# Optimization experiments

Measured on AMD Instinct MI355X. Metric: run time of the kernel, lower is better.

Reference implementation:

```python
import jax, jax.numpy as jnp
import numpy as np

N_NODES = 50000

def gcn_conv(x, src, dst, W, b, n_nodes):
    # PyG GCNConv: add self-loops, symmetric normalization D^-1/2 (A+I) D^-1/2, then bias
    loop = jnp.arange(n_nodes)
    s = jnp.concatenate([src, loop])
    d = jnp.concatenate([dst, loop])
    deg = jax.ops.segment_sum(jnp.ones(s.shape[0], x.dtype), d, num_segments=n_nodes)
    dinv = jnp.where(deg > 0, jax.lax.rsqrt(deg), 0.0)
    norm = dinv[s] * dinv[d]                      # [E+N]
    h = x @ W                                      # [N, out]
    msg = h[s] * norm[:, None]                     # gather + scale
    out = jax.ops.segment_sum(msg, d, num_segments=n_nodes)  # scatter-add
    return out + b

def setup_inputs() -> dict:
    key = jax.random.key(0)
    ks = jax.random.split(key, 8)
    x = jax.random.normal(ks[0], (N_NODES, 128), jnp.float32)
    edge_index = jax.random.randint(ks[1], (2, 800000), 0, N_NODES)
    def glorot(k, fan_in, fan_out):
        lim = np.sqrt(6.0 / (fan_in + fan_out)).astype(np.float32)
        return jax.random.uniform(k, (fan_in, fan_out), jnp.float32, -lim, lim)
    return {
        "x": x,
        "edge_index": edge_index,
        "conv_w1": glorot(ks[2], 128, 64), "conv_b1": jnp.zeros((64,), jnp.float32),
        "conv_w2": glorot(ks[3], 64, 64),  "conv_b2": jnp.zeros((64,), jnp.float32),
        "fc_w1": glorot(ks[4], 64, 32),    "fc_b1": jnp.zeros((32,), jnp.float32),
        "fc_w2": glorot(ks[5], 32, 1),     "fc_b2": jnp.zeros((1,), jnp.float32),
    }

def reference(x, edge_index, conv_w1, conv_b1, conv_w2, conv_b2, fc_w1, fc_b1, fc_w2, fc_b2):
    src, dst = edge_index[0], edge_index[1]
    h = jnp.tanh(gcn_conv(x, src, dst, conv_w1, conv_b1, N_NODES))
    h = jnp.tanh(gcn_conv(h, src, dst, conv_w2, conv_b2, N_NODES))
    h = jnp.tanh(h @ fc_w1 + fc_b1)  # dropout is identity at inference
    return h @ fc_w2 + fc_b2          # [N, 1]
```

## Files before the change

kernel.cpp:

```cpp
#include <hip/hip_runtime.h>
#include <math.h>

#define TPB 256
#define NBK_MAX 512
#define FILL_CAP 4096
#define SC_CH 16

typedef short bf16x8 __attribute__((ext_vector_type(8)));
typedef float f32x4 __attribute__((ext_vector_type(4)));

__device__ __forceinline__ unsigned short rne_bf16(float f) {
  unsigned u = __float_as_uint(f);
  return (unsigned short)((u + 0x7fffu + ((u >> 16) & 1u)) >> 16);
}
__device__ __forceinline__ float bf16_f(unsigned short v) {
  return __uint_as_float((unsigned)v << 16);
}

__global__ __launch_bounds__(TPB) void k_bcount(const int* __restrict__ dst,
                                                int* __restrict__ btot, int E, int NBK) {
  __shared__ int h[NBK_MAX];
  int tid = threadIdx.x, blk = blockIdx.x, G = gridDim.x;
  for (int b = tid; b < NBK; b += TPB) h[b] = 0;
  __syncthreads();
  int chunk = (E + G - 1) / G, lo = blk * chunk, hi = min(E, lo + chunk);
  for (int e = lo + tid; e < hi; e += TPB) atomicAdd(&h[dst[e] >> 7], 1);
  __syncthreads();
  for (int b = tid; b < NBK; b += TPB)
    if (h[b]) atomicAdd(&btot[b], h[b]);
}

__global__ __launch_bounds__(TPB) void k_bstart(const int* __restrict__ btot,
                                                int* __restrict__ bstart,
                                                int* __restrict__ gcur,
                                                int* __restrict__ rowptr,
                                                int NBK, int N, int E) {
  __shared__ int sc[TPB];
  int t = threadIdx.x;
  int i0 = 2 * t, i1 = 2 * t + 1;
  int a0 = (i0 < NBK) ? btot[i0] : 0;
  int a1 = (i1 < NBK) ? btot[i1] : 0;
  int s = a0 + a1;
  sc[t] = s;
  __syncthreads();
  for (int o = 1; o < TPB; o <<= 1) {
    int v = (t >= o) ? sc[t - o] : 0;
    __syncthreads();
    sc[t] += v;
    __syncthreads();
  }
  int excl = sc[t] - s;
  if (i0 < NBK) { bstart[i0] = excl;      gcur[i0] = excl; }
  if (i1 < NBK) { bstart[i1] = excl + a0; gcur[i1] = excl + a0; }
  if (t == 0) { bstart[NBK] = E; rowptr[N] = E; }
}

__global__ __launch_bounds__(TPB) void k_bscatter(const int* __restrict__ src,
                                                  const int* __restrict__ dst,
                                                  int* __restrict__ gcur,
                                                  unsigned* __restrict__ e2,
                                                  int E, int NBK) {
  __shared__ int h[NBK_MAX];
  __shared__ int base[NBK_MAX];
  int tid = threadIdx.x, blk = blockIdx.x, G = gridDim.x;
  int chunk = (E + G - 1) / G, lo = blk * chunk, hi = min(E, lo + chunk);
  for (int t0 = lo; t0 < hi; t0 += TPB * SC_CH) {
    int sv[SC_CH], dv[SC_CH];
    for (int b = tid; b < NBK; b += TPB) h[b] = 0;
    __syncthreads();
#pragma unroll
    for (int u = 0; u < SC_CH; ++u) {
      int e = t0 + u * TPB + tid;
      if (e < hi) {
        dv[u] = dst[e];
        sv[u] = src[e];
        atomicAdd(&h[dv[u] >> 7], 1);
      } else {
        dv[u] = -1;
      }
    }
    __syncthreads();
    for (int b = tid; b < NBK; b += TPB) {
      int c = h[b];
      base[b] = c ? atomicAdd(&gcur[b], c) : 0;
    }
    __syncthreads();
    for (int b = tid; b < NBK; b += TPB) h[b] = 0;
    __syncthreads();
#pragma unroll
    for (int u = 0; u < SC_CH; ++u) {
      if (dv[u] >= 0) {
        int bk = dv[u] >> 7;
        int r = atomicAdd(&h[bk], 1);
        e2[base[bk] + r] = ((unsigned)sv[u] << 7) | (unsigned)(dv[u] & 127);
      }
    }
    __syncthreads();
  }
}

__global__ __launch_bounds__(TPB) void k_build(const unsigned* __restrict__ e2,
                                               const int* __restrict__ bstart,
                                               int* __restrict__ rowptr,
                                               float* __restrict__ dinv,
                                               int* __restrict__ col, int N) {
  __shared__ int c[128], sc[128], cur[128];
  __shared__ int buf[FILL_CAP];
  int tid = threadIdx.x, b = blockIdx.x;
  int st = bstart[b], en = bstart[b + 1], len = en - st;
  if (tid < 128) c[tid] = 0;
  __syncthreads();
  for (int i = st + tid; i < en; i += TPB) atomicAdd(&c[e2[i] & 127u], 1);
  __syncthreads();
  if (tid < 128) sc[tid] = c[tid];
  __syncthreads();
  for (int o = 1; o < 128; o <<= 1) {
    int v = (tid >= o && tid < 128) ? sc[tid - o] : 0;
    __syncthreads();
    if (tid < 128) sc[tid] += v;
    __syncthreads();
  }
  if (tid < 128) {
    int excl = sc[tid] - c[tid];
    cur[tid] = excl;
    int node = b * 128 + tid;
    if (node < N) {
      rowptr[node] = st + excl;
      dinv[node] = rsqrtf((float)(c[tid] + 1));
    }
  }
  __syncthreads();
  if (len <= FILL_CAP) {
    for (int i = st + tid; i < en; i += TPB) {
      unsigned v = e2[i];
      int p = atomicAdd(&cur[v & 127u], 1);
      buf[p] = (int)(v >> 7);
    }
    __syncthreads();
    for (int i = tid; i < len; i += TPB) col[st + i] = buf[i];
  } else {
    for (int i = st + tid; i < en; i += TPB) {
      unsigned v = e2[i];
      int p = atomicAdd(&cur[v & 127u], 1);
      col[st + p] = (int)(v >> 7);
    }
  }
}

__global__ __launch_bounds__(TPB) void k_wsplit2(const float* __restrict__ W1,
                                                 const float* __restrict__ W2,
                                                 unsigned short* __restrict__ hi1,
                                                 unsigned short* __restrict__ lo1,
                                                 unsigned short* __restrict__ hi2,
                                                 unsigned short* __restrict__ lo2) {
  int i = blockIdx.x * TPB + threadIdx.x;
  if (i < 128 * 64) {
    int k = i >> 6, n = i & 63;
    float w = W1[i];
    unsigned short h = rne_bf16(w);
    hi1[n * 128 + k] = h;
    lo1[n * 128 + k] = rne_bf16(w - bf16_f(h));
  } else if (i < 128 * 64 + 64 * 64) {
    int j = i - 128 * 64;
    int k = j >> 6, n = j & 63;
    float w = W2[j];
    unsigned short h = rne_bf16(w);
    hi2[n * 64 + k] = h;
    lo2[n * 64 + k] = rne_bf16(w - bf16_f(h));
  }
}

template <int K, bool AF32>
__global__ __launch_bounds__(TPB) void k_mm(const void* __restrict__ Ap,
                                            const unsigned short* __restrict__ WThi,
                                            const unsigned short* __restrict__ WTlo,
                                            unsigned short* __restrict__ Hout, int N) {
  constexpr int P = K + 8;
  __shared__ unsigned short sHi[64 * P];
  __shared__ unsigned short sLo[64 * P];
  int tid = threadIdx.x;
  constexpr int CH = 64 * K / 8;
  for (int i = tid; i < CH; i += TPB) {
    int n = i / (K / 8), ko = i % (K / 8);
    *(int4*)(sHi + n * P + ko * 8) = *(const int4*)(WThi + n * K + ko * 8);
    *(int4*)(sLo + n * P + ko * 8) = *(const int4*)(WTlo + n * K + ko * 8);
  }
  __syncthreads();
  int wave = tid >> 6, lane = tid & 63;
  int oct = lane >> 4, l15 = lane & 15;
  int base = blockIdx.x * 64 + wave * 16;
  int arow = base + l15;
  if (arow >= N) arow = N - 1;
  f32x4 acc[4] = {};
#pragma unroll
  for (int s = 0; s < K / 32; ++s) {
    bf16x8 ahi, alo;
    if (AF32) {
      const float* ap = (const float*)Ap + (size_t)arow * K + s * 32 + oct * 8;
      float4 f0 = *(const float4*)ap;
      float4 f1 = *(const float4*)(ap + 4);
      float fv[8] = {f0.x, f0.y, f0.z, f0.w, f1.x, f1.y, f1.z, f1.w};
#pragma unroll
      for (int j = 0; j < 8; ++j) {
        unsigned short hb = rne_bf16(fv[j]);
        ahi[j] = (short)hb;
        alo[j] = (short)rne_bf16(fv[j] - bf16_f(hb));
      }
    } else {
      ahi = *(const bf16x8*)((const unsigned short*)Ap + (size_t)arow * K + s * 32 + oct * 8);
    }
#pragma unroll
    for (int t = 0; t < 4; ++t) {
      bf16x8 bhi = *(const bf16x8*)(sHi + (t * 16 + l15) * P + s * 32 + oct * 8);
      bf16x8 blo = *(const bf16x8*)(sLo + (t * 16 + l15) * P + s * 32 + oct * 8);
      acc[t] = __builtin_amdgcn_mfma_f32_16x16x32_bf16(ahi, bhi, acc[t], 0, 0, 0);
      acc[t] = __builtin_amdgcn_mfma_f32_16x16x32_bf16(ahi, blo, acc[t], 0, 0, 0);
      if (AF32)
        acc[t] = __builtin_amdgcn_mfma_f32_16x16x32_bf16(alo, bhi, acc[t], 0, 0, 0);
    }
  }
#pragma unroll
  for (int r = 0; r < 4; ++r) {
    int row = base + oct * 4 + r;
    if (row < N) {
#pragma unroll
      for (int t = 0; t < 4; ++t)
        Hout[(size_t)row * 64 + t * 16 + l15] = rne_bf16(acc[t][r]);
    }
  }
}

__device__ __forceinline__ float rl_f(float v, int l) {
  return __int_as_float(__builtin_amdgcn_readlane(__float_as_int(v), l));
}

__global__ __launch_bounds__(TPB) void k_agg(const unsigned short* __restrict__ H,
                                             const int* __restrict__ rowptr,
                                             const int* __restrict__ col,
                                             const float* __restrict__ dinv,
                                             const float* __restrict__ bias,
                                             unsigned short* __restrict__ OUT, int N) {
  int i = (blockIdx.x * TPB + threadIdx.x) >> 6;
  int lane = threadIdx.x & 63;
  if (i >= N) return;
  float di = dinv[i];
  float acc = bf16_f(H[((size_t)i << 6) + lane]) * di * di;
  int beg = rowptr[i], end = rowptr[i + 1];
  for (int c0 = beg; c0 < end; c0 += 64) {
    int m = end - c0;
    if (m > 64) m = 64;
    int jj = c0 + lane;
    int sv = col[jj < end ? jj : beg];
    float nv = di * dinv[sv];
    int t = 0;
    for (; t + 8 <= m; t += 8) {
      int s0 = __builtin_amdgcn_readlane(sv, t + 0);
      int s1 = __builtin_amdgcn_readlane(sv, t + 1);
      int s2 = __builtin_amdgcn_readlane(sv, t + 2);
      int s3 = __builtin_amdgcn_readlane(sv, t + 3);
      int s4 = __builtin_amdgcn_readlane(sv, t + 4);
      int s5 = __builtin_amdgcn_readlane(sv, t + 5);
      int s6 = __builtin_amdgcn_readlane(sv, t + 6);
      int s7 = __builtin_amdgcn_readlane(sv, t + 7);
      float h0 = bf16_f(H[((size_t)s0 << 6) + lane]);
      float h1 = bf16_f(H[((size_t)s1 << 6) + lane]);
      float h2 = bf16_f(H[((size_t)s2 << 6) + lane]);
      float h3 = bf16_f(H[((size_t)s3 << 6) + lane]);
      float h4 = bf16_f(H[((size_t)s4 << 6) + lane]);
      float h5 = bf16_f(H[((size_t)s5 << 6) + lane]);
      float h6 = bf16_f(H[((size_t)s6 << 6) + lane]);
      float h7 = bf16_f(H[((size_t)s7 << 6) + lane]);
      acc += h0 * rl_f(nv, t + 0);
      acc += h1 * rl_f(nv, t + 1);
      acc += h2 * rl_f(nv, t + 2);
      acc += h3 * rl_f(nv, t + 3);
      acc += h4 * rl_f(nv, t + 4);
      acc += h5 * rl_f(nv, t + 5);
      acc += h6 * rl_f(nv, t + 6);
      acc += h7 * rl_f(nv, t + 7);
    }
    if (t + 4 <= m) {
      int s0 = __builtin_amdgcn_readlane(sv, t + 0);
      int s1 = __builtin_amdgcn_readlane(sv, t + 1);
      int s2 = __builtin_amdgcn_readlane(sv, t + 2);
      int s3 = __builtin_amdgcn_readlane(sv, t + 3);
      float h0 = bf16_f(H[((size_t)s0 << 6) + lane]);
      float h1 = bf16_f(H[((size_t)s1 << 6) + lane]);
      float h2 = bf16_f(H[((size_t)s2 << 6) + lane]);
      float h3 = bf16_f(H[((size_t)s3 << 6) + lane]);
      acc += h0 * rl_f(nv, t + 0);
      acc += h1 * rl_f(nv, t + 1);
      acc += h2 * rl_f(nv, t + 2);
      acc += h3 * rl_f(nv, t + 3);
      t += 4;
    }
    for (; t < m; ++t) {
      int s = __builtin_amdgcn_readlane(sv, t);
      acc += bf16_f(H[((size_t)s << 6) + lane]) * rl_f(nv, t);
    }
  }
  acc += bias[lane];
  OUT[((size_t)i << 6) + lane] = rne_bf16(tanhf(acc));
}

__global__ __launch_bounds__(TPB) void k_fc(const unsigned short* __restrict__ A,
                                            const float* __restrict__ w1,
                                            const float* __restrict__ b1,
                                            const float* __restrict__ w2,
                                            const float* __restrict__ b2,
                                            float* __restrict__ out, int N) {
  __shared__ float sw1t[32 * 64];
  __shared__ float sb1[32];
  __shared__ float sw2[32];
  __shared__ float sA[128 * 65];
  int tid = threadIdx.x;
  for (int i = tid; i < 32 * 64; i += TPB) {
    int j = i >> 6, k = i & 63;
    sw1t[i] = w1[k * 32 + j];
  }
  if (tid < 32) { sb1[tid] = b1[tid]; sw2[tid] = w2[tid]; }
  int base = blockIdx.x * 128;
  for (int i = tid; i < 128 * 64; i += TPB) {
    int r = i >> 6, c = i & 63;
    int g = base + r;
    sA[r * 65 + c] = (g < N) ? bf16_f(A[(size_t)g * 64 + c]) : 0.f;
  }
  __syncthreads();
  int r = tid >> 1, q = tid & 1;
  int node = base + r;
  const float* arow = &sA[r * 65];
  float o = 0.f;
  for (int j = q * 16; j < q * 16 + 16; ++j) {
    float accj = sb1[j];
    const float* wrow = &sw1t[j * 64];
#pragma unroll 8
    for (int k = 0; k < 64; ++k) accj += arow[k] * wrow[k];
    o += tanhf(accj) * sw2[j];
  }
  o += __shfl_xor(o, 1);
  if (q == 0 && node < N) out[node] = o + b2[0];
}

extern "C" void kernel_launch(void* const* d_in, const int* in_sizes, int n_in,
                              void* d_out, int out_size, void* d_ws, size_t ws_size,
                              hipStream_t stream) {
  const float* x   = (const float*)d_in[0];
  const int*   ei  = (const int*)d_in[1];
  const float* w1  = (const float*)d_in[2];
  const float* b1  = (const float*)d_in[3];
  const float* w2  = (const float*)d_in[4];
  const float* b2  = (const float*)d_in[5];
  const float* fw1 = (const float*)d_in[6];
  const float* fb1 = (const float*)d_in[7];
  const float* fw2 = (const float*)d_in[8];
  const float* fb2 = (const float*)d_in[9];
  float* out = (float*)d_out;

  int N = in_sizes[0] / 128;
  int E = in_sizes[1] / 2;
  const int* src = ei;
  const int* dst = ei + E;

  const int G   = 256;
  const int NBK = (N + 127) / 128;

  char* p = (char*)d_ws;
  size_t off = 0;
  auto take = [&](size_t bytes) -> void* {
    void* r = p + off;
    off += (bytes + 255) & ~(size_t)255;
    return r;
  };
  int*            btot   = (int*)take((size_t)NBK * 4);
  int*            bstart = (int*)take((size_t)(NBK + 1) * 4);
  int*            gcur   = (int*)take((size_t)NBK * 4);
  int*            rowptr = (int*)take((size_t)(N + 1) * 4);
  float*          dinv   = (float*)take((size_t)N * 4);
  unsigned*       e2     = (unsigned*)take((size_t)E * 4);
  int*            col    = (int*)take((size_t)E * 4);
  unsigned short* wt1hi  = (unsigned short*)take(64 * 128 * 2);
  unsigned short* wt1lo  = (unsigned short*)take(64 * 128 * 2);
  unsigned short* wt2hi  = (unsigned short*)take(64 * 64 * 2);
  unsigned short* wt2lo  = (unsigned short*)take(64 * 64 * 2);
  unsigned short* h      = (unsigned short*)take((size_t)N * 64 * 2);
  unsigned short* a      = (unsigned short*)take((size_t)N * 64 * 2);
  (void)ws_size; (void)n_in; (void)out_size;

  hipMemsetAsync(btot, 0, (size_t)NBK * 4, stream);
  k_bcount<<<G, TPB, 0, stream>>>(dst, btot, E, NBK);
  k_bstart<<<1, TPB, 0, stream>>>(btot, bstart, gcur, rowptr, NBK, N, E);
  k_bscatter<<<G, TPB, 0, stream>>>(src, dst, gcur, e2, E, NBK);
  k_build<<<NBK, TPB, 0, stream>>>(e2, bstart, rowptr, dinv, col, N);

  k_wsplit2<<<48, TPB, 0, stream>>>(w1, w2, wt1hi, wt1lo, wt2hi, wt2lo);

  int gmm = (N + 63) / 64;
  k_mm<128, true><<<gmm, TPB, 0, stream>>>(x, wt1hi, wt1lo, h, N);
  k_agg<<<(N + 3) / 4, TPB, 0, stream>>>(h, rowptr, col, dinv, b1, a, N);
  k_mm<64, false><<<gmm, TPB, 0, stream>>>(a, wt2hi, wt2lo, h, N);
  k_agg<<<(N + 3) / 4, TPB, 0, stream>>>(h, rowptr, col, dinv, b2, a, N);
  k_fc<<<(N + 127) / 128, TPB, 0, stream>>>(a, fw1, fb1, fw2, fb2, out, N);
}
```

Before: 218.2 us.

## Fuse weight split into matmul, vectorize aggregation gather, fuse FC head into second aggregation

Removes the separate weight-split kernel: each matmul block now converts the fp32 weights to bf16 hi/lo pairs directly into shared memory. The aggregation kernel is restructured so each lane loads 4 bf16 features (8 bytes) and the wave handles 4 edges per step, followed by a cross-lane shuffle reduction. The second aggregation now runs as a persistent grid that also computes the FC layers, so the separate k_fc kernel and one intermediate write/read disappear. The costs are redundant weight conversion in every matmul block, extra shuffles, and per-group __syncthreads in the fused kernel.

```diff
diff --git a/kernel.cpp b/kernel.cpp
--- a/kernel.cpp
+++ b/kernel.cpp
@@ -16,6 +16,8 @@
 __device__ __forceinline__ float bf16_f(unsigned short v) {
   return __uint_as_float((unsigned)v << 16);
 }
+__device__ __forceinline__ float blo(unsigned u) { return __uint_as_float(u << 16); }
+__device__ __forceinline__ float bhi(unsigned u) { return __uint_as_float(u & 0xffff0000u); }
 
 __global__ __launch_bounds__(TPB) void k_bcount(const int* __restrict__ dst,
                                                 int* __restrict__ btot, int E, int NBK) {
@@ -147,43 +149,20 @@
   }
 }
 
-__global__ __launch_bounds__(TPB) void k_wsplit2(const float* __restrict__ W1,
-                                                 const float* __restrict__ W2,
-                                                 unsigned short* __restrict__ hi1,
-                                                 unsigned short* __restrict__ lo1,
-                                                 unsigned short* __restrict__ hi2,
-                                                 unsigned short* __restrict__ lo2) {
-  int i = blockIdx.x * TPB + threadIdx.x;
-  if (i < 128 * 64) {
-    int k = i >> 6, n = i & 63;
-    float w = W1[i];
-    unsigned short h = rne_bf16(w);
-    hi1[n * 128 + k] = h;
-    lo1[n * 128 + k] = rne_bf16(w - bf16_f(h));
-  } else if (i < 128 * 64 + 64 * 64) {
-    int j = i - 128 * 64;
-    int k = j >> 6, n = j & 63;
-    float w = W2[j];
-    unsigned short h = rne_bf16(w);
-    hi2[n * 64 + k] = h;
-    lo2[n * 64 + k] = rne_bf16(w - bf16_f(h));
-  }
-}
-
 template <int K, bool AF32>
 __global__ __launch_bounds__(TPB) void k_mm(const void* __restrict__ Ap,
-                                            const unsigned short* __restrict__ WThi,
-                                            const unsigned short* __restrict__ WTlo,
+                                            const float* __restrict__ W,
                                             unsigned short* __restrict__ Hout, int N) {
   constexpr int P = K + 8;
   __shared__ unsigned short sHi[64 * P];
   __shared__ unsigned short sLo[64 * P];
   int tid = threadIdx.x;
-  constexpr int CH = 64 * K / 8;
-  for (int i = tid; i < CH; i += TPB) {
-    int n = i / (K / 8), ko = i % (K / 8);
-    *(int4*)(sHi + n * P + ko * 8) = *(const int4*)(WThi + n * K + ko * 8);
-    *(int4*)(sLo + n * P + ko * 8) = *(const int4*)(WTlo + n * K + ko * 8);
+  for (int i = tid; i < K * 64; i += TPB) {
+    int k = i >> 6, n = i & 63;
+    float w = W[i];
+    unsigned short hb = rne_bf16(w);
+    sHi[n * P + k] = hb;
+    sLo[n * P + k] = rne_bf16(w - bf16_f(hb));
   }
   __syncthreads();
   int wave = tid >> 6, lane = tid & 63;
@@ -230,21 +209,18 @@
   }
 }
 
-__device__ __forceinline__ float rl_f(float v, int l) {
-  return __int_as_float(__builtin_amdgcn_readlane(__float_as_int(v), l));
-}
-
-__global__ __launch_bounds__(TPB) void k_agg(const unsigned short* __restrict__ H,
-                                             const int* __restrict__ rowptr,
-                                             const int* __restrict__ col,
-                                             const float* __restrict__ dinv,
-                                             const float* __restrict__ bias,
-                                             unsigned short* __restrict__ OUT, int N) {
-  int i = (blockIdx.x * TPB + threadIdx.x) >> 6;
+__device__ __forceinline__ float agg_node(int i, const unsigned short* __restrict__ H,
+                                          const int* __restrict__ rowptr,
+                                          const int* __restrict__ col,
+                                          const float* __restrict__ dinv,
+                                          float bfeat) {
   int lane = threadIdx.x & 63;
-  if (i >= N) return;
+  int q = lane & 15, ep = lane >> 4;
   float di = dinv[i];
-  float acc = bf16_f(H[((size_t)i << 6) + lane]) * di * di;
+  uint2 sf = *(const uint2*)(H + ((size_t)i << 6) + q * 4);
+  float w0 = (ep == 0) ? di * di : 0.f;
+  float ax = w0 * blo(sf.x), ay = w0 * bhi(sf.x);
+  float az = w0 * blo(sf.y), aw = w0 * bhi(sf.y);
   int beg = rowptr[i], end = rowptr[i + 1];
   for (int c0 = beg; c0 < end; c0 += 64) {
     int m = end - c0;
@@ -252,94 +228,109 @@
     int jj = c0 + lane;
     int sv = col[jj < end ? jj : beg];
     float nv = di * dinv[sv];
-    int t = 0;
-    for (; t + 8 <= m; t += 8) {
-      int s0 = __builtin_amdgcn_readlane(sv, t + 0);
-      int s1 = __builtin_amdgcn_readlane(sv, t + 1);
-      int s2 = __builtin_amdgcn_readlane(sv, t + 2);
-      int s3 = __builtin_amdgcn_readlane(sv, t + 3);
-      int s4 = __builtin_amdgcn_readlane(sv, t + 4);
-      int s5 = __builtin_amdgcn_readlane(sv, t + 5);
-      int s6 = __builtin_amdgcn_readlane(sv, t + 6);
-      int s7 = __builtin_amdgcn_readlane(sv, t + 7);
-      float h0 = bf16_f(H[((size_t)s0 << 6) + lane]);
-      float h1 = bf16_f(H[((size_t)s1 << 6) + lane]);
-      float h2 = bf16_f(H[((size_t)s2 << 6) + lane]);
-      float h3 = bf16_f(H[((size_t)s3 << 6) + lane]);
-      float h4 = bf16_f(H[((size_t)s4 << 6) + lane]);
-      float h5 = bf16_f(H[((size_t)s5 << 6) + lane]);
-      float h6 = bf16_f(H[((size_t)s6 << 6) + lane]);
-      float h7 = bf16_f(H[((size_t)s7 << 6) + lane]);
-      acc += h0 * rl_f(nv, t + 0);
-      acc += h1 * rl_f(nv, t + 1);
-      acc += h2 * rl_f(nv, t + 2);
-      acc += h3 * rl_f(nv, t + 3);
-      acc += h4 * rl_f(nv, t + 4);
-      acc += h5 * rl_f(nv, t + 5);
-      acc += h6 * rl_f(nv, t + 6);
-      acc += h7 * rl_f(nv, t + 7);
-    }
-    if (t + 4 <= m) {
-      int s0 = __builtin_amdgcn_readlane(sv, t + 0);
-      int s1 = __builtin_amdgcn_readlane(sv, t + 1);
-      int s2 = __builtin_amdgcn_readlane(sv, t + 2);
-      int s3 = __builtin_amdgcn_readlane(sv, t + 3);
-      float h0 = bf16_f(H[((size_t)s0 << 6) + lane]);
-      float h1 = bf16_f(H[((size_t)s1 << 6) + lane]);
-      float h2 = bf16_f(H[((size_t)s2 << 6) + lane]);
-      float h3 = bf16_f(H[((size_t)s3 << 6) + lane]);
-      acc += h0 * rl_f(nv, t + 0);
-      acc += h1 * rl_f(nv, t + 1);
-      acc += h2 * rl_f(nv, t + 2);
-      acc += h3 * rl_f(nv, t + 3);
-      t += 4;
-    }
-    for (; t < m; ++t) {
-      int s = __builtin_amdgcn_readlane(sv, t);
-      acc += bf16_f(H[((size_t)s << 6) + lane]) * rl_f(nv, t);
-    }
-  }
-  acc += bias[lane];
-  OUT[((size_t)i << 6) + lane] = rne_bf16(tanhf(acc));
-}
-
-__global__ __launch_bounds__(TPB) void k_fc(const unsigned short* __restrict__ A,
-                                            const float* __restrict__ w1,
-                                            const float* __restrict__ b1,
-                                            const float* __restrict__ w2,
-                                            const float* __restrict__ b2,
-                                            float* __restrict__ out, int N) {
+    for (int t = 0; t < m; t += 16) {
+      uint2 hv[4];
+      float wv[4];
+#pragma unroll
+      for (int g = 0; g < 4; ++g) {
+        int e = t + g * 4 + ep;
+        int s = __shfl(sv, e);
+        float w = __shfl(nv, e);
+        wv[g] = (e < m) ? w : 0.f;
+        hv[g] = *(const uint2*)(H + ((size_t)s << 6) + q * 4);
+      }
+#pragma unroll
+      for (int g = 0; g < 4; ++g) {
+        float w = wv[g];
+        ax += w * blo(hv[g].x);
+        ay += w * bhi(hv[g].x);
+        az += w * blo(hv[g].y);
+        aw += w * bhi(hv[g].y);
+      }
+    }
+  }
+#pragma unroll
+  for (int o = 16; o < 64; o <<= 1) {
+    ax += __shfl_xor(ax, o);
+    ay += __shfl_xor(ay, o);
+    az += __shfl_xor(az, o);
+    aw += __shfl_xor(aw, o);
+  }
+  int srcl = lane >> 2;
+  float v0 = __shfl(ax, srcl);
+  float v1 = __shfl(ay, srcl);
+  float v2 = __shfl(az, srcl);
+  float v3 = __shfl(aw, srcl);
+  float va = (lane & 1) ? v1 : v0;
+  float vb = (lane & 1) ? v3 : v2;
+  float v = (lane & 2) ? vb : va;
+  return tanhf(v + bfeat);
+}
+
+template <bool DOFC>
+__global__ __launch_bounds__(TPB) void k_agg(const unsigned short* __restrict__ H,
+                                             const int* __restrict__ rowptr,
+                                             const int* __restrict__ col,
+                                             const float* __restrict__ dinv,
+                                             const float* __restrict__ bias,
+                                             unsigned short* __restrict__ OUT,
+                                             const float* __restrict__ fw1,
+                                             const float* __restrict__ fb1,
+                                             const float* __restrict__ fw2,
+                                             const float* __restrict__ fb2,
+                                             float* __restrict__ fout, int N) {
   __shared__ float sw1t[32 * 64];
   __shared__ float sb1[32];
   __shared__ float sw2[32];
-  __shared__ float sA[128 * 65];
+  __shared__ float sA[4 * 64];
   int tid = threadIdx.x;
-  for (int i = tid; i < 32 * 64; i += TPB) {
-    int j = i >> 6, k = i & 63;
-    sw1t[i] = w1[k * 32 + j];
-  }
-  if (tid < 32) { sb1[tid] = b1[tid]; sw2[tid] = w2[tid]; }
-  int base = blockIdx.x * 128;
-  for (int i = tid; i < 128 * 64; i += TPB) {
-    int r = i >> 6, c = i & 63;
-    int g = base + r;
-    sA[r * 65 + c] = (g < N) ? bf16_f(A[(size_t)g * 64 + c]) : 0.f;
-  }
-  __syncthreads();
-  int r = tid >> 1, q = tid & 1;
-  int node = base + r;
-  const float* arow = &sA[r * 65];
-  float o = 0.f;
-  for (int j = q * 16; j < q * 16 + 16; ++j) {
-    float accj = sb1[j];
-    const float* wrow = &sw1t[j * 64];
-#pragma unroll 8
-    for (int k = 0; k < 64; ++k) accj += arow[k] * wrow[k];
-    o += tanhf(accj) * sw2[j];
-  }
-  o += __shfl_xor(o, 1);
-  if (q == 0 && node < N) out[node] = o + b2[0];
-}
+  int wid = tid >> 6, lane = tid & 63;
+  float bfeat = bias[lane];
+  if (DOFC) {
+    for (int i = tid; i < 32 * 64; i += TPB) {
+      int j = i >> 6, k = i & 63;
+      sw1t[i] = fw1[k * 32 + j];
+    }
+    if (tid < 32) { sb1[tid] = fb1[tid]; sw2[tid] = fw2[tid]; }
+    __syncthreads();
+  }
+  if (!DOFC) {
+    int i = (blockIdx.x * TPB + tid) >> 6;
+    if (i < N)
+      OUT[((size_t)i << 6) + lane] = rne_bf16(agg_node(i, H, rowptr, col, dinv, bfeat));
+    return;
+  }
+  int ngroups = (N + 3) / 4;
+  float b2v = fb2[0];
+  for (int grp = blockIdx.x; grp < ngroups; grp += gridDim.x) {
+    int i = grp * 4 + wid;
+    float aval = 0.f;
+    if (i < N) aval = agg_node(i, H, rowptr, col, dinv, bfeat);
+    sA[wid * 64 + lane] = aval;
+    __syncthreads();
+    if (tid < 128) {
+      int n = tid >> 5, j = tid & 31;
+      int node = grp * 4 + n;
+      if (node < N) {
+        float acc = sb1[j];
+        const float4* ar = (const float4*)(sA + n * 64);
+        const float* wr = sw1t + j * 64;
+#pragma unroll
+        for (int k4 = 0; k4 < 16; ++k4) {
+          float4 av = ar[k4];
+          acc += av.x * wr[4 * k4 + 0] + av.y * wr[4 * k4 + 1] +
+                 av.z * wr[4 * k4 + 2] + av.w * wr[4 * k4 + 3];
+        }
+        float t = tanhf(acc) * sw2[j];
+#pragma unroll
+        for (int o = 1; o < 32; o <<= 1) t += __shfl_xor(t, o);
+        if (j == 0) fout[node] = t + b2v;
+      }
+    }
+    __syncthreads();
+  }
+}
+
 
 extern "C" void kernel_launch(void* const* d_in, const int* in_sizes, int n_in,
                               void* d_out, int out_size, void* d_ws, size_t ws_size,
@@ -378,10 +369,6 @@
   float*          dinv   = (float*)take((size_t)N * 4);
   unsigned*       e2     = (unsigned*)take((size_t)E * 4);
   int*            col    = (int*)take((size_t)E * 4);
-  unsigned short* wt1hi  = (unsigned short*)take(64 * 128 * 2);
-  unsigned short* wt1lo  = (unsigned short*)take(64 * 128 * 2);
-  unsigned short* wt2hi  = (unsigned short*)take(64 * 64 * 2);
-  unsigned short* wt2lo  = (unsigned short*)take(64 * 64 * 2);
   unsigned short* h      = (unsigned short*)take((size_t)N * 64 * 2);
   unsigned short* a      = (unsigned short*)take((size_t)N * 64 * 2);
   (void)ws_size; (void)n_in; (void)out_size;
@@ -392,12 +379,12 @@
   k_bscatter<<<G, TPB, 0, stream>>>(src, dst, gcur, e2, E, NBK);
   k_build<<<NBK, TPB, 0, stream>>>(e2, bstart, rowptr, dinv, col, N);
 
-  k_wsplit2<<<48, TPB, 0, stream>>>(w1, w2, wt1hi, wt1lo, wt2hi, wt2lo);
-
   int gmm = (N + 63) / 64;
-  k_mm<128, true><<<gmm, TPB, 0, stream>>>(x, wt1hi, wt1lo, h, N);
-  k_agg<<<(N + 3) / 4, TPB, 0, stream>>>(h, rowptr, col, dinv, b1, a, N);
-  k_mm<64, false><<<gmm, TPB, 0, stream>>>(a, wt2hi, wt2lo, h, N);
-  k_agg<<<(N + 3) / 4, TPB, 0, stream>>>(h, rowptr, col, dinv, b2, a, N);
-  k_fc<<<(N + 127) / 128, TPB, 0, stream>>>(a, fw1, fb1, fw2, fb2, out, N);
-}
+  k_mm<128, true><<<gmm, TPB, 0, stream>>>(x, w1, h, N);
+  k_agg<false><<<(N + 3) / 4, TPB, 0, stream>>>(h, rowptr, col, dinv, b1, a,
+                                                nullptr, nullptr, nullptr, nullptr,
+                                                nullptr, N);
+  k_mm<64, false><<<gmm, TPB, 0, stream>>>(a, w2, h, N);
+  k_agg<true><<<1536, TPB, 0, stream>>>(h, rowptr, col, dinv, b2, nullptr,
+                                        fw1, fb1, fw2, fb2, out, N);
+}
```

After: 237.6 us. 1.09x slower.
